# Kernel tuning notes

Hardware: AMD Instinct MI355X
Metric: run time of the kernel (lower is better)

The kernel has to match this reference:

```python
import jax, jax.numpy as jnp
import numpy as np
import math

DIM = 1024
HEADS = 16
HEAD_DIM = DIM // HEADS
ROT = min(HEAD_DIM, 32)  # rotary_dim
B, S = 2, 1024


def setup_inputs() -> dict:
    key = jax.random.key(0)
    ks = jax.random.split(key, 32)
    lin = lambda k: jax.random.normal(k, (DIM, DIM), jnp.float32) * 0.02
    bias = lambda k: jax.random.normal(k, (DIM,), jnp.float32) * 0.01
    inp = {
        'real': jax.random.normal(ks[0], (B, S, DIM), jnp.float32),
        'imag': jax.random.normal(ks[1], (B, S, DIM), jnp.float32),
        'Wq_r': lin(ks[2]), 'bq_r': bias(ks[3]),
        'Wk_r': lin(ks[4]), 'bk_r': bias(ks[5]),
        'Wv_r': lin(ks[6]), 'bv_r': bias(ks[7]),
        'Wq_i': lin(ks[8]), 'bq_i': bias(ks[9]),
        'Wk_i': lin(ks[10]), 'bk_i': bias(ks[11]),
        'Wv_i': lin(ks[12]), 'bv_i': bias(ks[13]),
        'Wo_r': lin(ks[14]), 'bo_r': bias(ks[15]),
        'Wo_i': lin(ks[16]), 'bo_i': bias(ks[17]),
        'phase_shifts': jax.random.normal(ks[18], (HEADS, HEAD_DIM), jnp.float32) * 0.02,
        'ent': jnp.eye(HEADS, dtype=jnp.float32) + jax.random.normal(ks[19], (HEADS, HEADS), jnp.float32) * 0.01,
        'rot_freqs': (10000.0 ** (-jnp.arange(0, ROT, 2, dtype=jnp.float32) / ROT)),
        'strength': jnp.ones((1,), jnp.float32),
        'temp': jnp.ones((1,), jnp.float32),
    }
    return inp


def _fwd(real, imag, Wq_r, bq_r, Wk_r, bk_r, Wv_r, bv_r,
         Wq_i, bq_i, Wk_i, bk_i, Wv_i, bv_i,
         Wo_r, bo_r, Wo_i, bo_i,
         phase_shifts, ent, rot_freqs, strength, temp):
    b, s, _ = real.shape
    to_heads = lambda t: t.reshape(b, s, HEADS, HEAD_DIM).transpose(0, 2, 1, 3)  # bhsd
    lin = lambda x, W, bb: x @ W + bb

    q_r = to_heads(lin(real, Wq_r, bq_r))
    k_r = to_heads(lin(real, Wk_r, bk_r))
    v_r = to_heads(lin(real, Wv_r, bv_r))
    q_i = to_heads(lin(imag, Wq_i, bq_i))
    k_i = to_heads(lin(imag, Wk_i, bk_i))
    v_i = to_heads(lin(imag, Wv_i, bv_i))

    # rotary on first ROT dims (pairwise rotation)
    pos = jnp.arange(s, dtype=jnp.float32)
    emb = pos[:, None] * rot_freqs[None, :]           # [S, ROT/2]
    cos = jnp.cos(emb)[None, None]                    # [1,1,S,ROT/2]
    sin = jnp.sin(emb)[None, None]

    def rope(t):
        tr = t[..., :ROT].reshape(b, HEADS, s, ROT // 2, 2)
        r0 = tr[..., 0] * cos - tr[..., 1] * sin
        r1 = tr[..., 1] * cos + tr[..., 0] * sin
        rr = jnp.stack([r0, r1], axis=-1).reshape(b, HEADS, s, ROT)
        return jnp.concatenate([rr, t[..., ROT:]], axis=-1)

    q_r, k_r = rope(q_r), rope(k_r)
    q_i, k_i = rope(q_i), rope(k_i)

    # entanglement mixing across heads
    mix = lambda t: jnp.einsum('bhsd,hx->bxsd', t, ent)
    q_r, q_i, k_r, k_i = mix(q_r), mix(q_i), mix(k_r), mix(k_i)

    # per-head phase shift (complex rotation)
    pc = jnp.cos(phase_shifts)[None, :, None, :]      # [1,H,1,D]
    ps = jnp.sin(phase_shifts)[None, :, None, :]
    q_r, q_i = q_r * pc - q_i * ps, q_r * ps + q_i * pc
    k_r, k_i = k_r * pc - k_i * ps, k_r * ps + k_i * pc

    scale = 1.0 / math.sqrt(HEAD_DIM)
    attn_r = (jnp.einsum('bhqd,bhkd->bhqk', q_r, k_r) + jnp.einsum('bhqd,bhkd->bhqk', q_i, k_i)) * scale
    attn_i = (jnp.einsum('bhqd,bhkd->bhqk', q_i, k_r) - jnp.einsum('bhqd,bhkd->bhqk', q_r, k_i)) * scale
    attn_mag = jnp.sqrt(attn_r ** 2 + attn_i ** 2 + 1e-6)

    causal = jnp.triu(jnp.ones((s, s), dtype=bool), k=1)[None, None]
    attn_mag = jnp.where(causal, -jnp.inf, attn_mag)

    t = jnp.maximum(temp, 0.01)
    g = jax.nn.sigmoid(strength)
    attn = jax.nn.softmax(attn_mag * g / t, axis=-1)

    out_r = jnp.einsum('bhqk,bhkd->bhqd', attn, v_r).transpose(0, 2, 1, 3).reshape(b, s, DIM)
    out_i = jnp.einsum('bhqk,bhkd->bhqd', attn, v_i).transpose(0, 2, 1, 3).reshape(b, s, DIM)
    return lin(out_r, Wo_r, bo_r), lin(out_i, Wo_i, bo_i)


def reference(real, imag, Wq_r, bq_r, Wk_r, bk_r, Wv_r, bv_r,
              Wq_i, bq_i, Wk_i, bk_i, Wv_i, bv_i,
              Wo_r, bo_r, Wo_i, bo_i,
              phase_shifts, ent, rot_freqs, strength, temp):
    return _fwd(real, imag, Wq_r, bq_r, Wk_r, bk_r, Wv_r, bv_r,
                Wq_i, bq_i, Wk_i, bk_i, Wv_i, bv_i,
                Wo_r, bo_r, Wo_i, bo_i,
                phase_shifts, ent, rot_freqs, strength, temp)
```

## Files before the change

kernel.cpp:

```cpp
#include <hip/hip_runtime.h>
#include <stdint.h>

typedef unsigned short u16;
typedef __bf16 bf16x8 __attribute__((ext_vector_type(8)));
typedef float f32x4 __attribute__((ext_vector_type(4)));
typedef unsigned int u32x4 __attribute__((ext_vector_type(4)));

__device__ __forceinline__ u16 f2bf(float f) {
  uint32_t u = __float_as_uint(f);
  u += 0x7FFFu + ((u >> 16) & 1u);
  return (u16)(u >> 16);
}
__device__ __forceinline__ float bf2f(u16 h) {
  return __uint_as_float(((uint32_t)h) << 16);
}
__device__ __forceinline__ void gld16(const void* g, void* lds) {
  __builtin_amdgcn_global_load_lds(
      (const __attribute__((address_space(1))) uint32_t*)g,
      (__attribute__((address_space(3))) uint32_t*)lds, 16, 0, 0);
}
__device__ __forceinline__ f32x4 mfma16(u32x4 a, u32x4 b, f32x4 c) {
  return __builtin_amdgcn_mfma_f32_16x16x32_bf16(
      __builtin_bit_cast(bf16x8, a), __builtin_bit_cast(bf16x8, b), c, 0, 0, 0);
}

__global__ __launch_bounds__(256) void convx_kernel(const float* __restrict__ real,
                                                    const float* __restrict__ imag,
                                                    u16* __restrict__ Xr,
                                                    u16* __restrict__ Xi) {
  int u = blockIdx.x * 256 + threadIdx.x;
  int a = u >> 18;
  int r = u & 262143;
  int m = r >> 7, slot = r & 127;
  const float* src = (a ? imag : real) + (size_t)m * 1024 + slot * 8;
  int slot2 = (slot & ~7) | ((slot ^ m) & 7);
  u16* dst = (a ? Xi : Xr) + (size_t)m * 1024 + slot2 * 8;
  f32x4 v0 = *(const f32x4*)(src);
  f32x4 v1 = *(const f32x4*)(src + 4);
  union { u16 h[8]; u32x4 v; } o;
#pragma unroll
  for (int e = 0; e < 4; ++e) { o.h[e] = f2bf(v0[e]); o.h[4 + e] = f2bf(v1[e]); }
  *(u32x4*)dst = o.v;
}

__global__ __launch_bounds__(256) void convw_kernel(
    const float* __restrict__ w0, const float* __restrict__ w1,
    const float* __restrict__ w2, const float* __restrict__ w3,
    const float* __restrict__ w4, const float* __restrict__ w5,
    const float* __restrict__ w6, const float* __restrict__ w7,
    u16* __restrict__ WtAll) {
  __shared__ float Lt[64][65];
  int z = blockIdx.z;
  const float* W = (z == 0) ? w0 : (z == 1) ? w1 : (z == 2) ? w2 : (z == 3) ? w3
                 : (z == 4) ? w4 : (z == 5) ? w5 : (z == 6) ? w6 : w7;
  u16* Wt = WtAll + (size_t)z * (1024 * 1024);
  int tid = threadIdx.x;
  int n0 = blockIdx.x * 64, k0 = blockIdx.y * 64;
#pragma unroll
  for (int it = 0; it < 4; ++it) {
    int idx = it * 256 + tid;
    int kr = idx >> 4, nc = (idx & 15) * 4;
    f32x4 v = *(const f32x4*)(W + (size_t)(k0 + kr) * 1024 + n0 + nc);
#pragma unroll
    for (int e = 0; e < 4; ++e) Lt[kr][nc + e] = v[e];
  }
  __syncthreads();
#pragma unroll
  for (int it = 0; it < 2; ++it) {
    int idx = it * 256 + tid;
    int nr = idx >> 3, sl = idx & 7;
    union { u16 h[8]; u32x4 v; } o;
#pragma unroll
    for (int e = 0; e < 8; ++e) o.h[e] = f2bf(Lt[sl * 8 + e][nr]);
    int sl2 = sl ^ (nr & 7);
    *(u32x4*)(Wt + (size_t)(n0 + nr) * 1024 + k0 + sl2 * 8) = o.v;
  }
}

__device__ __forceinline__ void gemm128(const u16* __restrict__ A, const u16* __restrict__ W,
                                        const float* __restrict__ bias,
                                        u16* __restrict__ outB, float* __restrict__ outF) {
  __shared__ __align__(16) u16 As[128 * 64];
  __shared__ __align__(16) u16 Bs[128 * 64];
  int tid = threadIdx.x, l = tid & 63, w = tid >> 6;
  int lr = l & 15, lh = l >> 4;
  int m0 = blockIdx.y * 128, n0 = blockIdx.x * 128;
  int wr = w >> 1, wc = w & 1;
  f32x4 acc[4][4];
#pragma unroll
  for (int mi = 0; mi < 4; ++mi)
#pragma unroll
    for (int ni = 0; ni < 4; ++ni) acc[mi][ni] = f32x4{0.f, 0.f, 0.f, 0.f};

  for (int kt = 0; kt < 16; ++kt) {
#pragma unroll
    for (int c = 0; c < 4; ++c) {
      int chunk = c * 4 + w;
      int i = chunk * 64 + l;
      int row = i >> 3, off = i & 7;
      gld16(A + (size_t)(m0 + row) * 1024 + kt * 64 + off * 8, (char*)As + chunk * 1024);
      gld16(W + (size_t)(n0 + row) * 1024 + kt * 64 + off * 8, (char*)Bs + chunk * 1024);
    }
    __syncthreads();
#pragma unroll
    for (int kk = 0; kk < 2; ++kk) {
      u32x4 af[4], bf[4];
#pragma unroll
      for (int mi = 0; mi < 4; ++mi) {
        int row = wr * 64 + mi * 16 + lr;
        af[mi] = *(const u32x4*)((const char*)As + row * 128 +
                                 ((kk * 64 + lh * 16) ^ ((row & 7) << 4)));
      }
#pragma unroll
      for (int ni = 0; ni < 4; ++ni) {
        int row = wc * 64 + ni * 16 + lr;
        bf[ni] = *(const u32x4*)((const char*)Bs + row * 128 +
                                 ((kk * 64 + lh * 16) ^ ((row & 7) << 4)));
      }
#pragma unroll
      for (int mi = 0; mi < 4; ++mi)
#pragma unroll
        for (int ni = 0; ni < 4; ++ni)
          acc[mi][ni] = mfma16(af[mi], bf[ni], acc[mi][ni]);
    }
    __syncthreads();
  }
#pragma unroll
  for (int ni = 0; ni < 4; ++ni) {
    int col = n0 + wc * 64 + ni * 16 + lr;
    float bv = bias[col];
#pragma unroll
    for (int mi = 0; mi < 4; ++mi)
#pragma unroll
      for (int rr = 0; rr < 4; ++rr) {
        int row = m0 + wr * 64 + mi * 16 + 4 * lh + rr;
        float v = acc[mi][ni][rr] + bv;
        if (outF) outF[(size_t)row * 1024 + col] = v;
        else      outB[(size_t)row * 1024 + col] = f2bf(v);
      }
  }
}

__global__ __launch_bounds__(256) void gemm_proj_kernel(
    const u16* __restrict__ Xr, const u16* __restrict__ Xi, const u16* __restrict__ Wt,
    const float* b0, const float* b1, const float* b2,
    const float* b3, const float* b4, const float* b5,
    u16* __restrict__ qkv) {
  int z = blockIdx.z;
  const u16* A = (z < 3) ? Xr : Xi;
  const u16* W = Wt + (size_t)z * (1024 * 1024);
  const float* bias = (z == 0) ? b0 : (z == 1) ? b1 : (z == 2) ? b2
                    : (z == 3) ? b3 : (z == 4) ? b4 : b5;
  u16* out = qkv + (size_t)z * (2048 * 1024);
  gemm128(A, W, bias, out, nullptr);
}

__global__ __launch_bounds__(256) void gemm_out_kernel(
    const u16* __restrict__ O, const u16* __restrict__ Wt2,
    const float* br, const float* bi, float* __restrict__ dout) {
  int z = blockIdx.z;
  gemm128(O + (size_t)z * (2048 * 1024), Wt2 + (size_t)z * (1024 * 1024),
          z ? bi : br, nullptr, dout + (size_t)z * (2048 * 1024));
}

__global__ __launch_bounds__(256) void transform_kernel(
    const u16* __restrict__ qkv, const float* __restrict__ phase,
    const float* __restrict__ ent, const float* __restrict__ rotf,
    u16* __restrict__ Qr, u16* __restrict__ Qi, u16* __restrict__ Kr,
    u16* __restrict__ Ki, u16* __restrict__ Vr, u16* __restrict__ Vi) {
  __shared__ float Lqr[16][65], Lqi[16][65], Lkr[16][65], Lki[16][65];
  __shared__ float sent[256];
  int tid = threadIdx.x;
  int bs = blockIdx.x;
  int b = bs >> 10, s = bs & 1023;
  sent[tid] = ent[tid];
  const u16* qr_raw = qkv;
  const u16* kr_raw = qkv + (size_t)1 * 2048 * 1024;
  const u16* vr_raw = qkv + (size_t)2 * 2048 * 1024;
  const u16* qi_raw = qkv + (size_t)3 * 2048 * 1024;
  const u16* ki_raw = qkv + (size_t)4 * 2048 * 1024;
  const u16* vi_raw = qkv + (size_t)5 * 2048 * 1024;
  size_t rowoff = (size_t)bs * 1024;
#pragma unroll
  for (int it = 0; it < 2; ++it) {
    int u = it * 256 + tid;
    int hh = u >> 5, j = u & 31;
    int base = hh * 64 + 2 * j;
    uint32_t aqr = *(const uint32_t*)(qr_raw + rowoff + base);
    uint32_t aqi = *(const uint32_t*)(qi_raw + rowoff + base);
    uint32_t akr = *(const uint32_t*)(kr_raw + rowoff + base);
    uint32_t aki = *(const uint32_t*)(ki_raw + rowoff + base);
    float qr0 = bf2f((u16)aqr), qr1 = bf2f((u16)(aqr >> 16));
    float qi0 = bf2f((u16)aqi), qi1 = bf2f((u16)(aqi >> 16));
    float kr0 = bf2f((u16)akr), kr1 = bf2f((u16)(akr >> 16));
    float ki0 = bf2f((u16)aki), ki1 = bf2f((u16)(aki >> 16));
    if (j < 16) {
      float sn, cs;
      sincosf((float)s * rotf[j], &sn, &cs);
      float t0;
      t0 = qr0; qr0 = t0 * cs - qr1 * sn; qr1 = qr1 * cs + t0 * sn;
      t0 = qi0; qi0 = t0 * cs - qi1 * sn; qi1 = qi1 * cs + t0 * sn;
      t0 = kr0; kr0 = t0 * cs - kr1 * sn; kr1 = kr1 * cs + t0 * sn;
      t0 = ki0; ki0 = t0 * cs - ki1 * sn; ki1 = ki1 * cs + t0 * sn;
    }
    int d0 = 2 * j;
    Lqr[hh][d0] = qr0; Lqr[hh][d0 + 1] = qr1;
    Lqi[hh][d0] = qi0; Lqi[hh][d0 + 1] = qi1;
    Lkr[hh][d0] = kr0; Lkr[hh][d0 + 1] = kr1;
    Lki[hh][d0] = ki0; Lki[hh][d0 + 1] = ki1;
  }
  __syncthreads();
#pragma unroll
  for (int it = 0; it < 4; ++it) {
    int u = it * 256 + tid;
    int x = u >> 6, d = u & 63;
    float mqr = 0.f, mqi = 0.f, mkr = 0.f, mki = 0.f;
#pragma unroll
    for (int hh = 0; hh < 16; ++hh) {
      float e = sent[hh * 16 + x];
      mqr += Lqr[hh][d] * e; mqi += Lqi[hh][d] * e;
      mkr += Lkr[hh][d] * e; mki += Lki[hh][d] * e;
    }
    float ps_, pc_;
    sincosf(phase[x * 64 + d], &ps_, &pc_);
    float oqr = (mqr * pc_ - mqi * ps_) * 0.125f;
    float oqi = (mqr * ps_ + mqi * pc_) * 0.125f;
    float okr = mkr * pc_ - mki * ps_;
    float oki = mkr * ps_ + mki * pc_;
    size_t obase = ((size_t)(b * 16 + x) * 1024 + s) * 64;
    Qr[obase + d] = f2bf(oqr);
    Qi[obase + d] = f2bf(oqi);
    int dsw = (d & 7) | ((((d >> 3) ^ s) & 7) << 3);
    Kr[obase + dsw] = f2bf(okr);
    Ki[obase + dsw] = f2bf(oki);
  }
  {
    int u = tid;
    int comp = u >> 7, hh = (u >> 3) & 15, sl = u & 7;
    const u16* src = comp ? vi_raw : vr_raw;
    u16* dst = comp ? Vi : Vr;
    u32x4 vv = *(const u32x4*)(src + rowoff + hh * 64 + sl * 8);
    *(u32x4*)(dst + ((size_t)(b * 16 + hh) * 1024 + s) * 64 + sl * 8) = vv;
  }
}

__global__ __launch_bounds__(256) void transv_kernel(const u16* __restrict__ Vr,
                                                     const u16* __restrict__ Vi,
                                                     u16* __restrict__ VTr,
                                                     u16* __restrict__ VTi) {
  int bid = blockIdx.x;
  int comp = bid >> 9, bh = (bid >> 4) & 31, t = bid & 15;
  const u16* src = (comp ? Vi : Vr) + ((size_t)bh * 1024 + t * 64) * 64;
  u16* dst = (comp ? VTi : VTr) + (size_t)bh * 65536;
  __shared__ __align__(16) u16 Lt[64][72];
  int tid = threadIdx.x;
#pragma unroll
  for (int it = 0; it < 2; ++it) {
    int i = it * 256 + tid;
    int r = i >> 3, sl = i & 7;
    *(u32x4*)(&Lt[r][sl * 8]) = *(const u32x4*)(src + r * 64 + sl * 8);
  }
  __syncthreads();
#pragma unroll
  for (int it = 0; it < 2; ++it) {
    int i = it * 256 + tid;
    int d = i >> 3, sl = i & 7;
    union { u16 h[8]; u32x4 v; } o;
#pragma unroll
    for (int e = 0; e < 8; ++e) o.h[e] = Lt[sl * 8 + e][d];
    int sl2 = sl ^ (d & 7);
    *(u32x4*)(dst + (size_t)d * 1024 + t * 64 + sl2 * 8) = o.v;
  }
}

__global__ __launch_bounds__(256) void attn_kernel(
    const u16* __restrict__ Qr, const u16* __restrict__ Qi,
    const u16* __restrict__ Kr, const u16* __restrict__ Ki,
    const u16* __restrict__ VTr, const u16* __restrict__ VTi,
    const float* __restrict__ strength, const float* __restrict__ temp,
    u16* __restrict__ Or, u16* __restrict__ Oi) {
  __shared__ __align__(16) u16 smem[36864];
  char* sb = (char*)smem;
  const int PO = 65536;
  int tid = threadIdx.x, l = tid & 63, w = tid >> 6;
  int lr = l & 15, lh = l >> 4;
  int id = blockIdx.x;
  int x = id & 7, j = id >> 3;
  int bh = x + 8 * (j & 3);
  int qb = j >> 2;
  int b = bh >> 4, h = bh & 15;
  int q0 = qb * 64;
  float g = 1.f / (1.f + __expf(-strength[0]));
  float tt = fmaxf(temp[0], 0.01f);
  float gt = g / tt;

  size_t qbase = ((size_t)bh * 1024 + q0 + w * 16 + lr) * 64 + lh * 8;
  u32x4 qrF[2], qiF[2], nqrF[2];
#pragma unroll
  for (int kk = 0; kk < 2; ++kk) {
    qrF[kk] = *(const u32x4*)(Qr + qbase + kk * 32);
    qiF[kk] = *(const u32x4*)(Qi + qbase + kk * 32);
    nqrF[kk] = qrF[kk] ^ 0x80008000u;
  }
  f32x4 o_r[4], o_i[4];
#pragma unroll
  for (int n = 0; n < 4; ++n) { o_r[n] = f32x4{0,0,0,0}; o_i[n] = f32x4{0,0,0,0}; }
  float m_run[4], l_run[4];
#pragma unroll
  for (int rr = 0; rr < 4; ++rr) { m_run[rr] = -__builtin_inff(); l_run[rr] = 0.f; }

  auto stage = [&](int p, int t) {
    char* base = sb + p * 32768;
    if (w < 2) {
      const u16* Kp = (w ? Ki : Kr) + ((size_t)bh * 1024 + t * 64) * 64;
      char* dst = base + (w ? 8192 : 0);
#pragma unroll
      for (int c = 0; c < 8; ++c)
        gld16(Kp + c * 512 + l * 8, dst + c * 1024);
    } else {
      const u16* Vp = (w == 3 ? VTi : VTr) + (size_t)bh * 65536 + t * 64;
      char* dst = base + (w == 3 ? 24576 : 16384);
#pragma unroll
      for (int c = 0; c < 8; ++c) {
        int i = c * 64 + l;
        int d = i >> 3, off = i & 7;
        gld16(Vp + (size_t)d * 1024 + off * 8, dst + c * 1024);
      }
    }
  };

  stage(0, 0);
  __syncthreads();

  for (int t = 0; t <= qb; ++t) {
    int cur = t & 1;
    if (t < qb) stage(cur ^ 1, t + 1);
    char* kb = sb + cur * 32768;

    f32x4 sr[4], si[4];
#pragma unroll
    for (int n = 0; n < 4; ++n) { sr[n] = f32x4{0,0,0,0}; si[n] = f32x4{0,0,0,0}; }
#pragma unroll
    for (int kk = 0; kk < 2; ++kk) {
#pragma unroll
      for (int n = 0; n < 4; ++n) {
        int kv = n * 16 + lr;
        int xoff = (kk * 64 + lh * 16) ^ ((kv & 7) << 4);
        u32x4 fkr = *(const u32x4*)(kb + kv * 128 + xoff);
        u32x4 fki = *(const u32x4*)(kb + 8192 + kv * 128 + xoff);
        sr[n] = mfma16(qrF[kk], fkr, sr[n]);
        sr[n] = mfma16(qiF[kk], fki, sr[n]);
        si[n] = mfma16(qiF[kk], fkr, si[n]);
        si[n] = mfma16(nqrF[kk], fki, si[n]);
      }
    }

    float pl[4][4], pm[4];
#pragma unroll
    for (int rr = 0; rr < 4; ++rr) pm[rr] = -__builtin_inff();
    bool diag = (t == qb);
#pragma unroll
    for (int n = 0; n < 4; ++n)
#pragma unroll
      for (int rr = 0; rr < 4; ++rr) {
        float a = sr[n][rr], c = si[n][rr];
        float mag = sqrtf(a * a + c * c + 1e-6f) * gt;
        if (diag) {
          int colg = t * 64 + n * 16 + lr;
          int rowg = q0 + w * 16 + 4 * lh + rr;
          if (colg > rowg) mag = -__builtin_inff();
        }
        pl[n][rr] = mag;
        pm[rr] = fmaxf(pm[rr], mag);
      }
#pragma unroll
    for (int mk = 1; mk <= 8; mk <<= 1)
#pragma unroll
      for (int rr = 0; rr < 4; ++rr)
        pm[rr] = fmaxf(pm[rr], __shfl_xor(pm[rr], mk));
    float fr[4], rs[4];
#pragma unroll
    for (int rr = 0; rr < 4; ++rr) {
      float mnew = fmaxf(m_run[rr], pm[rr]);
      fr[rr] = __expf(m_run[rr] - mnew);
      m_run[rr] = mnew;
      rs[rr] = 0.f;
    }
#pragma unroll
    for (int n = 0; n < 4; ++n)
#pragma unroll
      for (int rr = 0; rr < 4; ++rr) {
        float p = __expf(pl[n][rr] - m_run[rr]);
        pl[n][rr] = p;
        rs[rr] += p;
      }
#pragma unroll
    for (int mk = 1; mk <= 8; mk <<= 1)
#pragma unroll
      for (int rr = 0; rr < 4; ++rr)
        rs[rr] += __shfl_xor(rs[rr], mk);
#pragma unroll
    for (int rr = 0; rr < 4; ++rr) l_run[rr] = l_run[rr] * fr[rr] + rs[rr];
#pragma unroll
    for (int n = 0; n < 4; ++n)
#pragma unroll
      for (int rr = 0; rr < 4; ++rr) { o_r[n][rr] *= fr[rr]; o_i[n][rr] *= fr[rr]; }

    char* pw = sb + PO + w * 2048;
#pragma unroll
    for (int n = 0; n < 4; ++n)
#pragma unroll
      for (int rr = 0; rr < 4; ++rr) {
        int row = 4 * lh + rr, col = n * 16 + lr;
        int by = row * 128 + ((col & 7) * 2) + ((((col >> 3) ^ row) & 7) << 4);
        *(u16*)(pw + by) = f2bf(pl[n][rr]);
      }
    u32x4 pf[2];
#pragma unroll
    for (int kk = 0; kk < 2; ++kk)
      pf[kk] = *(const u32x4*)(pw + lr * 128 + ((kk * 64 + lh * 16) ^ ((lr & 7) << 4)));
#pragma unroll
    for (int kk = 0; kk < 2; ++kk)
#pragma unroll
      for (int n = 0; n < 4; ++n) {
        int dl = n * 16 + lr;
        int xoff = (kk * 64 + lh * 16) ^ ((dl & 7) << 4);
        u32x4 fvr = *(const u32x4*)(kb + 16384 + dl * 128 + xoff);
        u32x4 fvi = *(const u32x4*)(kb + 24576 + dl * 128 + xoff);
        o_r[n] = mfma16(pf[kk], fvr, o_r[n]);
        o_i[n] = mfma16(pf[kk], fvi, o_i[n]);
      }
    __syncthreads();
  }
  float inv[4];
#pragma unroll
  for (int rr = 0; rr < 4; ++rr) inv[rr] = 1.f / l_run[rr];
#pragma unroll
  for (int n = 0; n < 4; ++n)
#pragma unroll
    for (int rr = 0; rr < 4; ++rr) {
      int s = q0 + w * 16 + 4 * lh + rr;
      int dl = n * 16 + lr;
      int dsw = (dl & 7) | ((((dl >> 3) ^ s) & 7) << 3);
      size_t oo = ((size_t)b * 1024 + s) * 1024 + h * 64 + dsw;
      Or[oo] = f2bf(o_r[n][rr] * inv[rr]);
      Oi[oo] = f2bf(o_i[n][rr] * inv[rr]);
    }
}

extern "C" void kernel_launch(void* const* d_in, const int* in_sizes, int n_in,
                              void* d_out, int out_size, void* d_ws, size_t ws_size,
                              hipStream_t stream) {
  (void)in_sizes; (void)n_in; (void)out_size; (void)ws_size;
  const float* real = (const float*)d_in[0];
  const float* imag = (const float*)d_in[1];
  const float* bq_r = (const float*)d_in[3];
  const float* bk_r = (const float*)d_in[5];
  const float* bv_r = (const float*)d_in[7];
  const float* bq_i = (const float*)d_in[9];
  const float* bk_i = (const float*)d_in[11];
  const float* bv_i = (const float*)d_in[13];
  const float* bo_r = (const float*)d_in[15];
  const float* bo_i = (const float*)d_in[17];
  const float* phase = (const float*)d_in[18];
  const float* ent = (const float*)d_in[19];
  const float* rotf = (const float*)d_in[20];
  const float* strength = (const float*)d_in[21];
  const float* temp = (const float*)d_in[22];

  u16* ws = (u16*)d_ws;
  const size_t M1 = 1024 * 1024, M2 = 2048 * 1024;
  u16* Xr  = ws;
  u16* Xi  = Xr + M2;
  u16* Wt  = Xi + M2;
  u16* qkv = Wt + 8 * M1;
  u16* Qr  = qkv + 6 * M2;
  u16* Qi  = Qr + M2;
  u16* Kr  = Qi + M2;
  u16* Ki  = Kr + M2;
  u16* Vr  = Ki + M2;
  u16* Vi  = Vr + M2;
  u16* VTr = Vi + M2;
  u16* VTi = VTr + M2;
  u16* Or  = VTi + M2;
  u16* Oi  = Or + M2;

  convx_kernel<<<2048, 256, 0, stream>>>(real, imag, Xr, Xi);
  convw_kernel<<<dim3(16, 16, 8), 256, 0, stream>>>(
      (const float*)d_in[2],  (const float*)d_in[4],  (const float*)d_in[6],
      (const float*)d_in[8],  (const float*)d_in[10], (const float*)d_in[12],
      (const float*)d_in[14], (const float*)d_in[16], Wt);
  gemm_proj_kernel<<<dim3(8, 16, 6), 256, 0, stream>>>(Xr, Xi, Wt, bq_r, bk_r, bv_r,
                                                       bq_i, bk_i, bv_i, qkv);
  transform_kernel<<<2048, 256, 0, stream>>>(qkv, phase, ent, rotf, Qr, Qi, Kr, Ki, Vr, Vi);
  transv_kernel<<<1024, 256, 0, stream>>>(Vr, Vi, VTr, VTi);
  attn_kernel<<<512, 256, 0, stream>>>(Qr, Qi, Kr, Ki, VTr, VTi, strength, temp, Or, Oi);
  gemm_out_kernel<<<dim3(8, 16, 2), 256, 0, stream>>>(Or, Wt + 6 * M1, bo_r, bo_i,
                                                      (float*)d_out);
}
```

Measured before the change: 159.1 us.

## Split attention KV range across four blocks and merge partials in combine kernel

The causal attention kernel now splits each query tile's key range into four chunks handled by separate blocks (2048 blocks instead of 512), with heavy query tiles scheduled first. Each block writes unnormalised bf16 partial outputs plus per-row max and sum to scratch buffers reused from earlier workspace, and a new combine kernel merges them with a log-sum-exp rescale. Double-buffered K/V staging is dropped for a single buffer with a sync per tile, cutting LDS use so more blocks fit per CU. This is meant to fix load imbalance and low occupancy in the causal loop, at the cost of an extra launch, extra global traffic, bf16 rounding of partials, and lost load/compute overlap.

```diff
diff --git a/kernel.cpp b/kernel.cpp
--- a/kernel.cpp
+++ b/kernel.cpp
@@ -278,30 +278,29 @@
     const u16* __restrict__ Kr, const u16* __restrict__ Ki,
     const u16* __restrict__ VTr, const u16* __restrict__ VTi,
     const float* __restrict__ strength, const float* __restrict__ temp,
-    u16* __restrict__ Or, u16* __restrict__ Oi) {
-  __shared__ __align__(16) u16 smem[36864];
+    u16* __restrict__ por0, u16* __restrict__ por1,
+    u16* __restrict__ por2, u16* __restrict__ por3,
+    u16* __restrict__ poi0, u16* __restrict__ poi1,
+    u16* __restrict__ poi2, u16* __restrict__ poi3,
+    float* __restrict__ Pm, float* __restrict__ Pl) {
+  __shared__ __align__(16) u16 smem[20480];
   char* sb = (char*)smem;
-  const int PO = 65536;
+  const int PO = 32768;
   int tid = threadIdx.x, l = tid & 63, w = tid >> 6;
   int lr = l & 15, lh = l >> 4;
   int id = blockIdx.x;
   int x = id & 7, j = id >> 3;
-  int bh = x + 8 * (j & 3);
-  int qb = j >> 2;
-  int b = bh >> 4, h = bh & 15;
+  int sp = j & 3, grp = j >> 2;
+  int bh = x + 8 * (grp & 3);
+  int qb = 15 - (grp >> 2);
+  int b_ = bh >> 4; (void)b_;
   int q0 = qb * 64;
-  float g = 1.f / (1.f + __expf(-strength[0]));
-  float tt = fmaxf(temp[0], 0.01f);
-  float gt = g / tt;
-
-  size_t qbase = ((size_t)bh * 1024 + q0 + w * 16 + lr) * 64 + lh * 8;
-  u32x4 qrF[2], qiF[2], nqrF[2];
-#pragma unroll
-  for (int kk = 0; kk < 2; ++kk) {
-    qrF[kk] = *(const u32x4*)(Qr + qbase + kk * 32);
-    qiF[kk] = *(const u32x4*)(Qi + qbase + kk * 32);
-    nqrF[kk] = qrF[kk] ^ 0x80008000u;
-  }
+  int nt = qb + 1;
+  int c = (nt + 3) >> 2;
+  int t0 = sp * c, t1 = min(nt, t0 + c);
+  u16* POr = (sp == 0) ? por0 : (sp == 1) ? por1 : (sp == 2) ? por2 : por3;
+  u16* POi = (sp == 0) ? poi0 : (sp == 1) ? poi1 : (sp == 2) ? poi2 : poi3;
+
   f32x4 o_r[4], o_i[4];
 #pragma unroll
   for (int n = 0; n < 4; ++n) { o_r[n] = f32x4{0,0,0,0}; o_i[n] = f32x4{0,0,0,0}; }
@@ -309,143 +308,202 @@
 #pragma unroll
   for (int rr = 0; rr < 4; ++rr) { m_run[rr] = -__builtin_inff(); l_run[rr] = 0.f; }
 
-  auto stage = [&](int p, int t) {
-    char* base = sb + p * 32768;
-    if (w < 2) {
-      const u16* Kp = (w ? Ki : Kr) + ((size_t)bh * 1024 + t * 64) * 64;
-      char* dst = base + (w ? 8192 : 0);
-#pragma unroll
-      for (int c = 0; c < 8; ++c)
-        gld16(Kp + c * 512 + l * 8, dst + c * 1024);
-    } else {
-      const u16* Vp = (w == 3 ? VTi : VTr) + (size_t)bh * 65536 + t * 64;
-      char* dst = base + (w == 3 ? 24576 : 16384);
-#pragma unroll
-      for (int c = 0; c < 8; ++c) {
-        int i = c * 64 + l;
-        int d = i >> 3, off = i & 7;
-        gld16(Vp + (size_t)d * 1024 + off * 8, dst + c * 1024);
+  if (t0 < t1) {
+    float g = 1.f / (1.f + __expf(-strength[0]));
+    float tt = fmaxf(temp[0], 0.01f);
+    float gt = g / tt;
+
+    size_t qbase = ((size_t)bh * 1024 + q0 + w * 16 + lr) * 64 + lh * 8;
+    u32x4 qrF[2], qiF[2], nqrF[2];
+#pragma unroll
+    for (int kk = 0; kk < 2; ++kk) {
+      qrF[kk] = *(const u32x4*)(Qr + qbase + kk * 32);
+      qiF[kk] = *(const u32x4*)(Qi + qbase + kk * 32);
+      nqrF[kk] = qrF[kk] ^ 0x80008000u;
+    }
+
+    for (int t = t0; t < t1; ++t) {
+      if (w < 2) {
+        const u16* Kp = (w ? Ki : Kr) + ((size_t)bh * 1024 + t * 64) * 64;
+        char* dst = sb + (w ? 8192 : 0);
+#pragma unroll
+        for (int cc = 0; cc < 8; ++cc)
+          gld16(Kp + cc * 512 + l * 8, dst + cc * 1024);
+      } else {
+        const u16* Vp = (w == 3 ? VTi : VTr) + (size_t)bh * 65536 + t * 64;
+        char* dst = sb + (w == 3 ? 24576 : 16384);
+#pragma unroll
+        for (int cc = 0; cc < 8; ++cc) {
+          int i = cc * 64 + l;
+          int d = i >> 3, off = i & 7;
+          gld16(Vp + (size_t)d * 1024 + off * 8, dst + cc * 1024);
+        }
       }
-    }
-  };
-
-  stage(0, 0);
-  __syncthreads();
-
-  for (int t = 0; t <= qb; ++t) {
-    int cur = t & 1;
-    if (t < qb) stage(cur ^ 1, t + 1);
-    char* kb = sb + cur * 32768;
-
-    f32x4 sr[4], si[4];
-#pragma unroll
-    for (int n = 0; n < 4; ++n) { sr[n] = f32x4{0,0,0,0}; si[n] = f32x4{0,0,0,0}; }
-#pragma unroll
-    for (int kk = 0; kk < 2; ++kk) {
-#pragma unroll
-      for (int n = 0; n < 4; ++n) {
-        int kv = n * 16 + lr;
-        int xoff = (kk * 64 + lh * 16) ^ ((kv & 7) << 4);
-        u32x4 fkr = *(const u32x4*)(kb + kv * 128 + xoff);
-        u32x4 fki = *(const u32x4*)(kb + 8192 + kv * 128 + xoff);
-        sr[n] = mfma16(qrF[kk], fkr, sr[n]);
-        sr[n] = mfma16(qiF[kk], fki, sr[n]);
-        si[n] = mfma16(qiF[kk], fkr, si[n]);
-        si[n] = mfma16(nqrF[kk], fki, si[n]);
+      __syncthreads();
+
+      f32x4 sr[4], si[4];
+#pragma unroll
+      for (int n = 0; n < 4; ++n) { sr[n] = f32x4{0,0,0,0}; si[n] = f32x4{0,0,0,0}; }
+#pragma unroll
+      for (int kk = 0; kk < 2; ++kk) {
+#pragma unroll
+        for (int n = 0; n < 4; ++n) {
+          int kv = n * 16 + lr;
+          int xoff = (kk * 64 + lh * 16) ^ ((kv & 7) << 4);
+          u32x4 fkr = *(const u32x4*)(sb + kv * 128 + xoff);
+          u32x4 fki = *(const u32x4*)(sb + 8192 + kv * 128 + xoff);
+          sr[n] = mfma16(qrF[kk], fkr, sr[n]);
+          sr[n] = mfma16(qiF[kk], fki, sr[n]);
+          si[n] = mfma16(qiF[kk], fkr, si[n]);
+          si[n] = mfma16(nqrF[kk], fki, si[n]);
+        }
       }
-    }
-
-    float pl[4][4], pm[4];
-#pragma unroll
-    for (int rr = 0; rr < 4; ++rr) pm[rr] = -__builtin_inff();
-    bool diag = (t == qb);
-#pragma unroll
-    for (int n = 0; n < 4; ++n)
+
+      float pl[4][4], pm[4];
+#pragma unroll
+      for (int rr = 0; rr < 4; ++rr) pm[rr] = -__builtin_inff();
+      bool diag = (t == qb);
+#pragma unroll
+      for (int n = 0; n < 4; ++n)
+#pragma unroll
+        for (int rr = 0; rr < 4; ++rr) {
+          float a = sr[n][rr], cc = si[n][rr];
+          float mag = sqrtf(a * a + cc * cc + 1e-6f) * gt;
+          if (diag) {
+            int colg = t * 64 + n * 16 + lr;
+            int rowg = q0 + w * 16 + 4 * lh + rr;
+            if (colg > rowg) mag = -__builtin_inff();
+          }
+          pl[n][rr] = mag;
+          pm[rr] = fmaxf(pm[rr], mag);
+        }
+#pragma unroll
+      for (int mk = 1; mk <= 8; mk <<= 1)
+#pragma unroll
+        for (int rr = 0; rr < 4; ++rr)
+          pm[rr] = fmaxf(pm[rr], __shfl_xor(pm[rr], mk));
+      float fr[4], rs[4];
 #pragma unroll
       for (int rr = 0; rr < 4; ++rr) {
-        float a = sr[n][rr], c = si[n][rr];
-        float mag = sqrtf(a * a + c * c + 1e-6f) * gt;
-        if (diag) {
-          int colg = t * 64 + n * 16 + lr;
-          int rowg = q0 + w * 16 + 4 * lh + rr;
-          if (colg > rowg) mag = -__builtin_inff();
+        float mnew = fmaxf(m_run[rr], pm[rr]);
+        fr[rr] = __expf(m_run[rr] - mnew);
+        m_run[rr] = mnew;
+        rs[rr] = 0.f;
+      }
+#pragma unroll
+      for (int n = 0; n < 4; ++n)
+#pragma unroll
+        for (int rr = 0; rr < 4; ++rr) {
+          float p = __expf(pl[n][rr] - m_run[rr]);
+          pl[n][rr] = p;
+          rs[rr] += p;
         }
-        pl[n][rr] = mag;
-        pm[rr] = fmaxf(pm[rr], mag);
-      }
-#pragma unroll
-    for (int mk = 1; mk <= 8; mk <<= 1)
-#pragma unroll
-      for (int rr = 0; rr < 4; ++rr)
-        pm[rr] = fmaxf(pm[rr], __shfl_xor(pm[rr], mk));
-    float fr[4], rs[4];
+#pragma unroll
+      for (int mk = 1; mk <= 8; mk <<= 1)
+#pragma unroll
+        for (int rr = 0; rr < 4; ++rr)
+          rs[rr] += __shfl_xor(rs[rr], mk);
+#pragma unroll
+      for (int rr = 0; rr < 4; ++rr) l_run[rr] = l_run[rr] * fr[rr] + rs[rr];
+#pragma unroll
+      for (int n = 0; n < 4; ++n)
+#pragma unroll
+        for (int rr = 0; rr < 4; ++rr) { o_r[n][rr] *= fr[rr]; o_i[n][rr] *= fr[rr]; }
+
+      char* pw = sb + PO + w * 2048;
+#pragma unroll
+      for (int n = 0; n < 4; ++n)
+#pragma unroll
+        for (int rr = 0; rr < 4; ++rr) {
+          int row = 4 * lh + rr, col = n * 16 + lr;
+          int by = row * 128 + ((col & 7) * 2) + ((((col >> 3) ^ row) & 7) << 4);
+          *(u16*)(pw + by) = f2bf(pl[n][rr]);
+        }
+      u32x4 pf[2];
+#pragma unroll
+      for (int kk = 0; kk < 2; ++kk)
+        pf[kk] = *(const u32x4*)(pw + lr * 128 + ((kk * 64 + lh * 16) ^ ((lr & 7) << 4)));
+#pragma unroll
+      for (int kk = 0; kk < 2; ++kk)
+#pragma unroll
+        for (int n = 0; n < 4; ++n) {
+          int dl = n * 16 + lr;
+          int xoff = (kk * 64 + lh * 16) ^ ((dl & 7) << 4);
+          u32x4 fvr = *(const u32x4*)(sb + 16384 + dl * 128 + xoff);
+          u32x4 fvi = *(const u32x4*)(sb + 24576 + dl * 128 + xoff);
+          o_r[n] = mfma16(pf[kk], fvr, o_r[n]);
+          o_i[n] = mfma16(pf[kk], fvi, o_i[n]);
+        }
+      __syncthreads();
+    }
+  }
+
+  size_t pbase = ((size_t)bh * 1024 + q0 + w * 16 + 4 * lh) * 64;
+#pragma unroll
+  for (int n = 0; n < 4; ++n)
 #pragma unroll
     for (int rr = 0; rr < 4; ++rr) {
-      float mnew = fmaxf(m_run[rr], pm[rr]);
-      fr[rr] = __expf(m_run[rr] - mnew);
-      m_run[rr] = mnew;
-      rs[rr] = 0.f;
-    }
-#pragma unroll
-    for (int n = 0; n < 4; ++n)
-#pragma unroll
-      for (int rr = 0; rr < 4; ++rr) {
-        float p = __expf(pl[n][rr] - m_run[rr]);
-        pl[n][rr] = p;
-        rs[rr] += p;
-      }
-#pragma unroll
-    for (int mk = 1; mk <= 8; mk <<= 1)
-#pragma unroll
-      for (int rr = 0; rr < 4; ++rr)
-        rs[rr] += __shfl_xor(rs[rr], mk);
-#pragma unroll
-    for (int rr = 0; rr < 4; ++rr) l_run[rr] = l_run[rr] * fr[rr] + rs[rr];
-#pragma unroll
-    for (int n = 0; n < 4; ++n)
-#pragma unroll
-      for (int rr = 0; rr < 4; ++rr) { o_r[n][rr] *= fr[rr]; o_i[n][rr] *= fr[rr]; }
-
-    char* pw = sb + PO + w * 2048;
-#pragma unroll
-    for (int n = 0; n < 4; ++n)
-#pragma unroll
-      for (int rr = 0; rr < 4; ++rr) {
-        int row = 4 * lh + rr, col = n * 16 + lr;
-        int by = row * 128 + ((col & 7) * 2) + ((((col >> 3) ^ row) & 7) << 4);
-        *(u16*)(pw + by) = f2bf(pl[n][rr]);
-      }
-    u32x4 pf[2];
-#pragma unroll
-    for (int kk = 0; kk < 2; ++kk)
-      pf[kk] = *(const u32x4*)(pw + lr * 128 + ((kk * 64 + lh * 16) ^ ((lr & 7) << 4)));
-#pragma unroll
-    for (int kk = 0; kk < 2; ++kk)
-#pragma unroll
-      for (int n = 0; n < 4; ++n) {
-        int dl = n * 16 + lr;
-        int xoff = (kk * 64 + lh * 16) ^ ((dl & 7) << 4);
-        u32x4 fvr = *(const u32x4*)(kb + 16384 + dl * 128 + xoff);
-        u32x4 fvi = *(const u32x4*)(kb + 24576 + dl * 128 + xoff);
-        o_r[n] = mfma16(pf[kk], fvr, o_r[n]);
-        o_i[n] = mfma16(pf[kk], fvi, o_i[n]);
-      }
-    __syncthreads();
-  }
-  float inv[4];
-#pragma unroll
-  for (int rr = 0; rr < 4; ++rr) inv[rr] = 1.f / l_run[rr];
-#pragma unroll
-  for (int n = 0; n < 4; ++n)
+      POr[pbase + rr * 64 + n * 16 + lr] = f2bf(o_r[n][rr]);
+      POi[pbase + rr * 64 + n * 16 + lr] = f2bf(o_i[n][rr]);
+    }
+  if (lr == 0) {
+    size_t mbase = (size_t)sp * 32768 + (size_t)bh * 1024 + q0 + w * 16 + 4 * lh;
 #pragma unroll
     for (int rr = 0; rr < 4; ++rr) {
-      int s = q0 + w * 16 + 4 * lh + rr;
-      int dl = n * 16 + lr;
-      int dsw = (dl & 7) | ((((dl >> 3) ^ s) & 7) << 3);
-      size_t oo = ((size_t)b * 1024 + s) * 1024 + h * 64 + dsw;
-      Or[oo] = f2bf(o_r[n][rr] * inv[rr]);
-      Oi[oo] = f2bf(o_i[n][rr] * inv[rr]);
-    }
+      Pm[mbase + rr] = m_run[rr];
+      Pl[mbase + rr] = l_run[rr];
+    }
+  }
+}
+
+__global__ __launch_bounds__(256) void combine_kernel(
+    const u16* __restrict__ por0, const u16* __restrict__ por1,
+    const u16* __restrict__ por2, const u16* __restrict__ por3,
+    const u16* __restrict__ poi0, const u16* __restrict__ poi1,
+    const u16* __restrict__ poi2, const u16* __restrict__ poi3,
+    const float* __restrict__ Pm, const float* __restrict__ Pl,
+    u16* __restrict__ Or, u16* __restrict__ Oi) {
+  int bid = blockIdx.x;
+  int bh = bid >> 4, rg = bid & 15;
+  int b = bh >> 4, h = bh & 15;
+  int tid = threadIdx.x;
+  int row = tid >> 2, q = tid & 3;
+  int s = rg * 64 + row;
+  size_t ro = (size_t)bh * 1024 + s;
+  float m0 = Pm[ro], m1 = Pm[ro + 32768], m2 = Pm[ro + 65536], m3 = Pm[ro + 98304];
+  float M = fmaxf(fmaxf(m0, m1), fmaxf(m2, m3));
+  float e0 = __expf(m0 - M), e1 = __expf(m1 - M);
+  float e2 = __expf(m2 - M), e3 = __expf(m3 - M);
+  float lt = Pl[ro] * e0 + Pl[ro + 32768] * e1 + Pl[ro + 65536] * e2 + Pl[ro + 98304] * e3;
+  float inv = 1.f / lt;
+  float c0 = e0 * inv, c1 = e1 * inv, c2 = e2 * inv, c3 = e3 * inv;
+  size_t obase = ro * 64;
+#pragma unroll
+  for (int g = 0; g < 2; ++g) {
+    int d = q * 16 + g * 8;
+    union { u16 h[8]; u32x4 v; } a0, a1, a2, a3;
+    union { u16 h[8]; u32x4 v; } outr, outi;
+    a0.v = *(const u32x4*)(por0 + obase + d);
+    a1.v = *(const u32x4*)(por1 + obase + d);
+    a2.v = *(const u32x4*)(por2 + obase + d);
+    a3.v = *(const u32x4*)(por3 + obase + d);
+#pragma unroll
+    for (int e = 0; e < 8; ++e)
+      outr.h[e] = f2bf(c0 * bf2f(a0.h[e]) + c1 * bf2f(a1.h[e]) +
+                       c2 * bf2f(a2.h[e]) + c3 * bf2f(a3.h[e]));
+    a0.v = *(const u32x4*)(poi0 + obase + d);
+    a1.v = *(const u32x4*)(poi1 + obase + d);
+    a2.v = *(const u32x4*)(poi2 + obase + d);
+    a3.v = *(const u32x4*)(poi3 + obase + d);
+#pragma unroll
+    for (int e = 0; e < 8; ++e)
+      outi.h[e] = f2bf(c0 * bf2f(a0.h[e]) + c1 * bf2f(a1.h[e]) +
+                       c2 * bf2f(a2.h[e]) + c3 * bf2f(a3.h[e]));
+    int slot2 = (d >> 3) ^ (s & 7);
+    size_t oo = ((size_t)b * 1024 + s) * 1024 + h * 64 + slot2 * 8;
+    *(u32x4*)(Or + oo) = outr.v;
+    *(u32x4*)(Oi + oo) = outi.v;
+  }
 }
 
 extern "C" void kernel_launch(void* const* d_in, const int* in_sizes, int n_in,
@@ -484,6 +542,16 @@
   u16* VTi = VTr + M2;
   u16* Or  = VTi + M2;
   u16* Oi  = Or + M2;
+  u16* por0 = qkv;
+  u16* por1 = qkv + M2;
+  u16* por2 = qkv + 2 * M2;
+  u16* por3 = qkv + 3 * M2;
+  u16* poi0 = qkv + 4 * M2;
+  u16* poi1 = qkv + 5 * M2;
+  u16* poi2 = Vr;
+  u16* poi3 = Vi;
+  float* Pm = (float*)Xr;
+  float* Pl = Pm + 131072;
 
   convx_kernel<<<2048, 256, 0, stream>>>(real, imag, Xr, Xi);
   convw_kernel<<<dim3(16, 16, 8), 256, 0, stream>>>(
@@ -494,7 +562,11 @@
                                                        bq_i, bk_i, bv_i, qkv);
   transform_kernel<<<2048, 256, 0, stream>>>(qkv, phase, ent, rotf, Qr, Qi, Kr, Ki, Vr, Vi);
   transv_kernel<<<1024, 256, 0, stream>>>(Vr, Vi, VTr, VTi);
-  attn_kernel<<<512, 256, 0, stream>>>(Qr, Qi, Kr, Ki, VTr, VTi, strength, temp, Or, Oi);
+  attn_kernel<<<2048, 256, 0, stream>>>(Qr, Qi, Kr, Ki, VTr, VTi, strength, temp,
+                                        por0, por1, por2, por3,
+                                        poi0, poi1, poi2, poi3, Pm, Pl);
+  combine_kernel<<<512, 256, 0, stream>>>(por0, por1, por2, por3,
+                                          poi0, poi1, poi2, poi3, Pm, Pl, Or, Oi);
   gemm_out_kernel<<<dim3(8, 16, 2), 256, 0, stream>>>(Or, Wt + 6 * M1, bo_r, bo_i,
                                                       (float*)d_out);
 }
```

Result: no change. 157.5 us (-1.0%).
